# Kernel optimization log

Hardware: AMD Instinct MI355X
Metric: run time of the kernel (lower is better)

The kernel has to match this reference:

```python
import jax, jax.numpy as jnp
import numpy as np

EPS = 1e-12  # matches torch.nn.functional.normalize eps


def _normalize(x):
    n = jnp.sqrt(jnp.sum(x * x, axis=-1, keepdims=True))
    return x / jnp.maximum(n, EPS)


def setup_inputs() -> dict:
    key = jax.random.key(0)
    k1, k2, k3 = jax.random.split(key, 3)
    B, C, D = 1024, 32768, 512
    embeddings = jax.random.normal(k1, (B, D), dtype=jnp.float32)
    proxies = jax.random.normal(k2, (C, D), dtype=jnp.float32) / 8.0
    labels = jax.random.randint(k3, (B,), 0, C, dtype=jnp.int64)
    return {"embeddings": embeddings, "proxies": proxies, "labels": labels}


def reference(embeddings, proxies, labels):
    # batch: [B, D], P: [C, D], both scaled to norm 3
    batch = 3.0 * _normalize(embeddings)
    P = 3.0 * _normalize(proxies)

    # Squared euclidean distances to ALL proxies via the expansion
    # ||b - p||^2 = ||b||^2 + ||p||^2 - 2 b.p  -> [B, C]
    b_sq = jnp.sum(batch * batch, axis=-1, keepdims=True)      # [B, 1]
    p_sq = jnp.sum(P * P, axis=-1)                             # [C]
    dist = b_sq + p_sq[None, :] - 2.0 * (batch @ P.T)          # [B, C]

    B = batch.shape[0]
    rows = jnp.arange(B)
    pos_dist = dist[rows, labels]                              # [B]

    # logsumexp over negatives: mask out the positive class per row
    neg_scores = jnp.where(
        jnp.arange(dist.shape[1])[None, :] == labels[:, None],
        -jnp.inf,
        -dist,
    )
    neg_lse = jax.nn.logsumexp(neg_scores, axis=1)             # [B]

    return jnp.mean(pos_dist + neg_lse)
```

## Files before the change

kernel.cpp:

```cpp
#include <hip/hip_runtime.h>
#include <hip/hip_fp8.h>
#include <stdint.h>

#define D_DIM 512
#define B_ROWS 1024
#define C_ROWS 32768
#define NBLK (C_ROWS / 128)

typedef __attribute__((ext_vector_type(4))) float floatx4;

#define GLOBAL_AS __attribute__((address_space(1)))
#define LDS_AS __attribute__((address_space(3)))

__device__ inline void async_copy16(const unsigned char* g, unsigned char* l) {
    __builtin_amdgcn_global_load_lds((const GLOBAL_AS void*)g, (LDS_AS void*)l, 16, 0, 0);
}

__device__ inline unsigned char f2fp8(float x) {
    __hip_fp8_e4m3 t(x);
    return t.__x;
}
__device__ inline float fp8tof(unsigned char v) {
    __hip_fp8_e4m3 t;
    t.__x = v;
    return (float)t;
}

__global__ void norm_rows_kernel(const float* __restrict__ prox,
                                 const float* __restrict__ emb,
                                 unsigned char* __restrict__ Pq,
                                 unsigned char* __restrict__ Aq,
                                 float* __restrict__ rowsum,
                                 float* __restrict__ acc,
                                 unsigned* __restrict__ ticket) {
    if (blockIdx.x == 0) {
        for (int i = threadIdx.x; i < B_ROWS; i += 256) rowsum[i] = 0.f;
        if (threadIdx.x == 0) { *acc = 0.f; *ticket = 0u; }
    }
    const int wid = threadIdx.x >> 6;
    const int lane = threadIdx.x & 63;
    int row = blockIdx.x * 4 + wid;
    const float* src;
    unsigned char* dst;
    if (row < C_ROWS) {
        src = prox; dst = Pq;
    } else {
        row -= C_ROWS;
        src = emb; dst = Aq;
    }

    const float4* p = (const float4*)(src + (size_t)row * D_DIM + lane * 8);
    float4 v0 = p[0];
    float4 v1 = p[1];
    float ss = v0.x * v0.x + v0.y * v0.y + v0.z * v0.z + v0.w * v0.w +
               v1.x * v1.x + v1.y * v1.y + v1.z * v1.z + v1.w * v1.w;
#pragma unroll
    for (int off = 1; off < 64; off <<= 1) ss += __shfl_xor(ss, off);
    const float s = 3.0f * rsqrtf(ss);

    unsigned char q[8];
    q[0] = f2fp8(v0.x * s); q[1] = f2fp8(v0.y * s);
    q[2] = f2fp8(v0.z * s); q[3] = f2fp8(v0.w * s);
    q[4] = f2fp8(v1.x * s); q[5] = f2fp8(v1.y * s);
    q[6] = f2fp8(v1.z * s); q[7] = f2fp8(v1.w * s);
    uint2 packed;
    packed.x = (unsigned)q[0] | ((unsigned)q[1] << 8) |
               ((unsigned)q[2] << 16) | ((unsigned)q[3] << 24);
    packed.y = (unsigned)q[4] | ((unsigned)q[5] << 8) |
               ((unsigned)q[6] << 16) | ((unsigned)q[7] << 24);
    *(uint2*)(dst + (size_t)row * D_DIM + lane * 8) = packed;
}

__global__ void __launch_bounds__(256, 3)
gemm_lse_kernel(const unsigned char* __restrict__ A,
                const unsigned char* __restrict__ Bm,
                float* __restrict__ rowsum) {
    __shared__ unsigned char sA[128 * 128];
    __shared__ unsigned char sB[128 * 128];
    __shared__ float red[128];

    const int tid = threadIdx.x;
    const int wid = tid >> 6;
    const int lane = tid & 63;
    const int n0 = blockIdx.x * 128;
    const int m0 = blockIdx.y * 128;

    if (tid < 128) red[tid] = 0.f;

    const int r8 = lane >> 3;
    const int pg = lane & 7;
    const int gl = (pg - r8) & 7;
    const unsigned char* gA = A + (size_t)(m0 + wid * 32 + r8) * D_DIM + gl * 16;
    const unsigned char* gB = Bm + (size_t)(n0 + wid * 32 + r8) * D_DIM + gl * 16;
    unsigned char* lA = &sA[wid * 32 * 128 + lane * 16];
    unsigned char* lB = &sB[wid * 32 * 128 + lane * 16];

    const int wm = (wid >> 1) * 64;
    const int wn = (wid & 1) * 64;
    const int fr = lane & 15;
    const int quad = lane >> 4;

    floatx4 acc[4][4];
    const floatx4 zero = {0.f, 0.f, 0.f, 0.f};
#pragma unroll
    for (int i = 0; i < 4; ++i)
#pragma unroll
        for (int j = 0; j < 4; ++j) acc[i][j] = zero;

    for (int c = 0; c < 4; ++c) {
        const int kb = c * 128;
#pragma unroll
        for (int j = 0; j < 4; ++j) {
            async_copy16(gA + kb + j * 8 * D_DIM, lA + j * 8 * 128);
            async_copy16(gB + kb + j * 8 * D_DIM, lB + j * 8 * 128);
        }
        __syncthreads();

#pragma unroll
        for (int s = 0; s < 4; ++s) {
            const int off = (((2 * s + (quad >> 1) + fr) & 7) * 16) + (quad & 1) * 8;
            long af[4], bf[4];
#pragma unroll
            for (int t = 0; t < 4; ++t) {
                af[t] = *(const long*)&sA[(wm + t * 16 + fr) * 128 + off];
                bf[t] = *(const long*)&sB[(wn + t * 16 + fr) * 128 + off];
            }
#pragma unroll
            for (int ti = 0; ti < 4; ++ti)
#pragma unroll
                for (int tj = 0; tj < 4; ++tj)
                    acc[ti][tj] = __builtin_amdgcn_mfma_f32_16x16x32_fp8_fp8(
                        af[ti], bf[tj], acc[ti][tj], 0, 0, 0);
        }
        __syncthreads();
    }

#pragma unroll
    for (int ti = 0; ti < 4; ++ti) {
        float rs[4] = {0.f, 0.f, 0.f, 0.f};
#pragma unroll
        for (int tj = 0; tj < 4; ++tj)
#pragma unroll
            for (int r = 0; r < 4; ++r)
                rs[r] += __expf(2.0f * acc[ti][tj][r]);
#pragma unroll
        for (int r = 0; r < 4; ++r) {
            rs[r] += __shfl_xor(rs[r], 1);
            rs[r] += __shfl_xor(rs[r], 2);
            rs[r] += __shfl_xor(rs[r], 4);
            rs[r] += __shfl_xor(rs[r], 8);
        }
        if (fr == 0) {
#pragma unroll
            for (int r = 0; r < 4; ++r)
                atomicAdd(&red[wm + ti * 16 + quad * 4 + r], rs[r]);
        }
    }
    __syncthreads();
    if (tid < 128) atomicAdd(&rowsum[m0 + tid], red[tid]);
}

__global__ void finalize_kernel(const float* __restrict__ rowsum,
                                const unsigned char* __restrict__ A,
                                const unsigned char* __restrict__ Bm,
                                const int* __restrict__ labels,
                                float* __restrict__ acc,
                                unsigned* __restrict__ ticket,
                                float* __restrict__ out) {
    __shared__ float r4[4];
    const int tid = threadIdx.x;
    const int wid = tid >> 6;
    const int lane = tid & 63;
    const int b = blockIdx.x * 4 + wid;

    const int l = labels[b];
    uint2 ua = *(const uint2*)(A + (size_t)b * D_DIM + lane * 8);
    uint2 ub = *(const uint2*)(Bm + (size_t)l * D_DIM + lane * 8);
    const unsigned char* au = (const unsigned char*)&ua;
    const unsigned char* bu = (const unsigned char*)&ub;
    float d = 0.f;
#pragma unroll
    for (int j = 0; j < 8; ++j) d += fp8tof(au[j]) * fp8tof(bu[j]);
#pragma unroll
    for (int off = 1; off < 64; off <<= 1) d += __shfl_xor(d, off);

    if (lane == 0) {
        float p2 = 2.0f * d;
        r4[wid] = logf(rowsum[b] - __expf(p2)) - p2;
    }
    __syncthreads();
    if (tid == 0) {
        float bl = r4[0] + r4[1] + r4[2] + r4[3];
        atomicAdd(acc, bl);
        __threadfence();
        unsigned t = atomicAdd(ticket, 1u);
        if (t == 255u) {
            float total = atomicAdd(acc, 0.f);
            out[0] = total / (float)B_ROWS;
        }
    }
}

extern "C" void kernel_launch(void* const* d_in, const int* in_sizes, int n_in,
                              void* d_out, int out_size, void* d_ws, size_t ws_size,
                              hipStream_t stream) {
    const float* emb = (const float*)d_in[0];
    const float* prox = (const float*)d_in[1];
    const int* labels = (const int*)d_in[2];
    float* out = (float*)d_out;

    char* ws = (char*)d_ws;
    unsigned char* Pq = (unsigned char*)ws;
    unsigned char* Aq = Pq + (size_t)C_ROWS * D_DIM;
    float* rowsum = (float*)(Aq + (size_t)B_ROWS * D_DIM);
    float* acc = rowsum + B_ROWS;
    unsigned* ticket = (unsigned*)(acc + 1);

    norm_rows_kernel<<<(C_ROWS + B_ROWS) / 4, 256, 0, stream>>>(
        prox, emb, Pq, Aq, rowsum, acc, ticket);
    gemm_lse_kernel<<<dim3(NBLK, B_ROWS / 128), 256, 0, stream>>>(Aq, Pq, rowsum);
    finalize_kernel<<<B_ROWS / 4, 256, 0, stream>>>(
        rowsum, Aq, Pq, labels, acc, ticket, out);
}
```

Before: 142.2 us.

## Pre-swizzle A into MFMA fragment layout and load from registers, not LDS

The normalization kernel now writes the quantized embeddings in a layout that matches the MFMA fragments. The GEMM can then read A fragments straight from global memory into registers, double-buffered one k-step ahead, so A no longer goes through LDS. The B tile grows to a 256-wide K chunk, which halves the number of sync rounds, and the launch bound rises to 4 blocks per CU because LDS use drops. In exchange, A is now loaded per wave from global or L2 instead of being shared through LDS, and register pressure rises.

```diff
diff --git a/kernel.cpp b/kernel.cpp
--- a/kernel.cpp
+++ b/kernel.cpp
@@ -25,6 +25,7 @@
     t.__x = v;
     return (float)t;
 }
+
 
 __global__ void norm_rows_kernel(const float* __restrict__ prox,
                                  const float* __restrict__ emb,
@@ -41,12 +42,12 @@
     const int lane = threadIdx.x & 63;
     int row = blockIdx.x * 4 + wid;
     const float* src;
-    unsigned char* dst;
-    if (row < C_ROWS) {
-        src = prox; dst = Pq;
+    const bool is_prox = (row < C_ROWS);
+    if (is_prox) {
+        src = prox;
     } else {
         row -= C_ROWS;
-        src = emb; dst = Aq;
+        src = emb;
     }
 
     const float4* p = (const float4*)(src + (size_t)row * D_DIM + lane * 8);
@@ -68,38 +69,44 @@
                ((unsigned)q[2] << 16) | ((unsigned)q[3] << 24);
     packed.y = (unsigned)q[4] | ((unsigned)q[5] << 8) |
                ((unsigned)q[6] << 16) | ((unsigned)q[7] << 24);
-    *(uint2*)(dst + (size_t)row * D_DIM + lane * 8) = packed;
-}
-
-__global__ void __launch_bounds__(256, 3)
-gemm_lse_kernel(const unsigned char* __restrict__ A,
+
+    if (is_prox) {
+        *(uint2*)(Pq + (size_t)row * D_DIM + lane * 8) = packed;
+    } else {
+        const size_t u = ((size_t)(row >> 4) * 16 + (lane >> 2)) * 64 +
+                         (lane & 3) * 16 + (row & 15);
+        *(uint2*)(Aq + u * 8) = packed;
+    }
+}
+
+__global__ void __launch_bounds__(256, 4)
+gemm_lse_kernel(const unsigned char* __restrict__ Afrag,
                 const unsigned char* __restrict__ Bm,
                 float* __restrict__ rowsum) {
-    __shared__ unsigned char sA[128 * 128];
-    __shared__ unsigned char sB[128 * 128];
+    __shared__ unsigned char sB[128 * 256];
     __shared__ float red[128];
 
     const int tid = threadIdx.x;
     const int wid = tid >> 6;
     const int lane = tid & 63;
     const int n0 = blockIdx.x * 128;
-    const int m0 = blockIdx.y * 128;
+    const int m0t = blockIdx.y * 8;
 
     if (tid < 128) red[tid] = 0.f;
 
-    const int r8 = lane >> 3;
-    const int pg = lane & 7;
-    const int gl = (pg - r8) & 7;
-    const unsigned char* gA = A + (size_t)(m0 + wid * 32 + r8) * D_DIM + gl * 16;
-    const unsigned char* gB = Bm + (size_t)(n0 + wid * 32 + r8) * D_DIM + gl * 16;
-    unsigned char* lA = &sA[wid * 32 * 128 + lane * 16];
-    unsigned char* lB = &sB[wid * 32 * 128 + lane * 16];
-
-    const int wm = (wid >> 1) * 64;
+    const int r4 = lane >> 4;
+    const int pg = lane & 15;
+    unsigned char* lB = &sB[wid * 32 * 256 + lane * 16];
+
+    const int wmt = (wid >> 1) * 4;
+    const int wm = wmt * 16;
     const int wn = (wid & 1) * 64;
     const int fr = lane & 15;
     const int quad = lane >> 4;
 
+    const unsigned char* Abase =
+        Afrag + ((size_t)(m0t + wmt) * 16 * 64 + lane) * 8;
+
     floatx4 acc[4][4];
     const floatx4 zero = {0.f, 0.f, 0.f, 0.f};
 #pragma unroll
@@ -107,30 +114,43 @@
 #pragma unroll
         for (int j = 0; j < 4; ++j) acc[i][j] = zero;
 
-    for (int c = 0; c < 4; ++c) {
-        const int kb = c * 128;
-#pragma unroll
-        for (int j = 0; j < 4; ++j) {
-            async_copy16(gA + kb + j * 8 * D_DIM, lA + j * 8 * 128);
-            async_copy16(gB + kb + j * 8 * D_DIM, lB + j * 8 * 128);
+    long afb[2][4];
+#pragma unroll
+    for (int t = 0; t < 4; ++t)
+        afb[0][t] = *(const long*)(Abase + t * 8192);
+
+    for (int c = 0; c < 2; ++c) {
+#pragma unroll
+        for (int j = 0; j < 8; ++j) {
+            const int row = wid * 32 + j * 4 + r4;
+            const int gl = (pg - row) & 15;
+            async_copy16(Bm + (size_t)(n0 + row) * D_DIM + c * 256 + gl * 16,
+                         lB + j * 4 * 256);
         }
         __syncthreads();
 
 #pragma unroll
-        for (int s = 0; s < 4; ++s) {
-            const int off = (((2 * s + (quad >> 1) + fr) & 7) * 16) + (quad & 1) * 8;
-            long af[4], bf[4];
-#pragma unroll
-            for (int t = 0; t < 4; ++t) {
-                af[t] = *(const long*)&sA[(wm + t * 16 + fr) * 128 + off];
-                bf[t] = *(const long*)&sB[(wn + t * 16 + fr) * 128 + off];
+        for (int s = 0; s < 8; ++s) {
+            const int sidx = c * 8 + s;
+            const int cur = sidx & 1;
+            if (sidx < 15) {
+#pragma unroll
+                for (int t = 0; t < 4; ++t)
+                    afb[cur ^ 1][t] =
+                        *(const long*)(Abase + t * 8192 + (sidx + 1) * 512);
             }
+            const int off =
+                ((2 * s + (quad >> 1) + fr) & 15) * 16 + (quad & 1) * 8;
+            long bf[4];
+#pragma unroll
+            for (int t = 0; t < 4; ++t)
+                bf[t] = *(const long*)&sB[(wn + t * 16 + fr) * 256 + off];
 #pragma unroll
             for (int ti = 0; ti < 4; ++ti)
 #pragma unroll
                 for (int tj = 0; tj < 4; ++tj)
                     acc[ti][tj] = __builtin_amdgcn_mfma_f32_16x16x32_fp8_fp8(
-                        af[ti], bf[tj], acc[ti][tj], 0, 0, 0);
+                        afb[cur][ti], bf[tj], acc[ti][tj], 0, 0, 0);
         }
         __syncthreads();
     }
@@ -157,25 +177,27 @@
         }
     }
     __syncthreads();
-    if (tid < 128) atomicAdd(&rowsum[m0 + tid], red[tid]);
+    if (tid < 128) atomicAdd(&rowsum[m0t * 16 + tid], red[tid]);
 }
 
 __global__ void finalize_kernel(const float* __restrict__ rowsum,
-                                const unsigned char* __restrict__ A,
-                                const unsigned char* __restrict__ Bm,
+                                const unsigned char* __restrict__ Afrag,
+                                const unsigned char* __restrict__ Pq,
                                 const int* __restrict__ labels,
                                 float* __restrict__ acc,
                                 unsigned* __restrict__ ticket,
                                 float* __restrict__ out) {
-    __shared__ float r4[4];
+    __shared__ float r4s[4];
     const int tid = threadIdx.x;
     const int wid = tid >> 6;
     const int lane = tid & 63;
     const int b = blockIdx.x * 4 + wid;
 
     const int l = labels[b];
-    uint2 ua = *(const uint2*)(A + (size_t)b * D_DIM + lane * 8);
-    uint2 ub = *(const uint2*)(Bm + (size_t)l * D_DIM + lane * 8);
+    const size_t u = ((size_t)(b >> 4) * 16 + (lane >> 2)) * 64 +
+                     (lane & 3) * 16 + (b & 15);
+    uint2 ua = *(const uint2*)(Afrag + u * 8);
+    uint2 ub = *(const uint2*)(Pq + (size_t)l * D_DIM + lane * 8);
     const unsigned char* au = (const unsigned char*)&ua;
     const unsigned char* bu = (const unsigned char*)&ub;
     float d = 0.f;
@@ -186,11 +208,11 @@
 
     if (lane == 0) {
         float p2 = 2.0f * d;
-        r4[wid] = logf(rowsum[b] - __expf(p2)) - p2;
+        r4s[wid] = logf(rowsum[b] - __expf(p2)) - p2;
     }
     __syncthreads();
     if (tid == 0) {
-        float bl = r4[0] + r4[1] + r4[2] + r4[3];
+        float bl = r4s[0] + r4s[1] + r4s[2] + r4s[3];
         atomicAdd(acc, bl);
         __threadfence();
         unsigned t = atomicAdd(ticket, 1u);
```

Result: slower. 157.2 us (+10.6%).

## Pre-tile fp8 operands into MFMA fragment layout and replace atomics with partial sums

Applied to the files above, without the earlier changes.

The normalization kernel now writes quantized rows directly in a tiled layout that matches the MFMA fragment order, so the GEMM loads contiguous 16-byte chunks and reads 16-byte vectors from LDS with no swizzle arithmetic. Global atomicAdd into rowsum is replaced by per-block partial sums written to a workspace buffer, which the finalize kernel reduces. Launch bounds go from 3 to 4 blocks per CU. The change adds a larger partial buffer and ties every consumer to the new layout.

```diff
diff --git a/kernel.cpp b/kernel.cpp
--- a/kernel.cpp
+++ b/kernel.cpp
@@ -8,6 +8,7 @@
 #define NBLK (C_ROWS / 128)
 
 typedef __attribute__((ext_vector_type(4))) float floatx4;
+typedef __attribute__((ext_vector_type(2))) long longx2;
 
 #define GLOBAL_AS __attribute__((address_space(1)))
 #define LDS_AS __attribute__((address_space(3)))
@@ -26,17 +27,14 @@
     return (float)t;
 }
 
+
 __global__ void norm_rows_kernel(const float* __restrict__ prox,
                                  const float* __restrict__ emb,
                                  unsigned char* __restrict__ Pq,
                                  unsigned char* __restrict__ Aq,
-                                 float* __restrict__ rowsum,
                                  float* __restrict__ acc,
                                  unsigned* __restrict__ ticket) {
-    if (blockIdx.x == 0) {
-        for (int i = threadIdx.x; i < B_ROWS; i += 256) rowsum[i] = 0.f;
-        if (threadIdx.x == 0) { *acc = 0.f; *ticket = 0u; }
-    }
+    if (blockIdx.x == 0 && threadIdx.x == 0) { *acc = 0.f; *ticket = 0u; }
     const int wid = threadIdx.x >> 6;
     const int lane = threadIdx.x & 63;
     int row = blockIdx.x * 4 + wid;
@@ -68,35 +66,31 @@
                ((unsigned)q[2] << 16) | ((unsigned)q[3] << 24);
     packed.y = (unsigned)q[4] | ((unsigned)q[5] << 8) |
                ((unsigned)q[6] << 16) | ((unsigned)q[7] << 24);
-    *(uint2*)(dst + (size_t)row * D_DIM + lane * 8) = packed;
-}
-
-__global__ void __launch_bounds__(256, 3)
-gemm_lse_kernel(const unsigned char* __restrict__ A,
-                const unsigned char* __restrict__ Bm,
-                float* __restrict__ rowsum) {
-    __shared__ unsigned char sA[128 * 128];
-    __shared__ unsigned char sB[128 * 128];
+
+    const size_t u = ((size_t)(row >> 4) * 8 + (lane >> 3)) * 64 +
+                     (lane & 3) * 16 + (row & 15);
+    *(uint2*)(dst + u * 16 + ((lane >> 2) & 1) * 8) = packed;
+}
+
+__global__ void __launch_bounds__(256, 4)
+gemm_lse_kernel(const unsigned char* __restrict__ Aq,
+                const unsigned char* __restrict__ Bq,
+                float* __restrict__ part) {
+    __shared__ unsigned char sA[16384];
+    __shared__ unsigned char sB[16384];
     __shared__ float red[128];
 
     const int tid = threadIdx.x;
     const int wid = tid >> 6;
     const int lane = tid & 63;
-    const int n0 = blockIdx.x * 128;
-    const int m0 = blockIdx.y * 128;
+    const int n0t = blockIdx.x * 8;
+    const int m0t = blockIdx.y * 8;
 
     if (tid < 128) red[tid] = 0.f;
 
-    const int r8 = lane >> 3;
-    const int pg = lane & 7;
-    const int gl = (pg - r8) & 7;
-    const unsigned char* gA = A + (size_t)(m0 + wid * 32 + r8) * D_DIM + gl * 16;
-    const unsigned char* gB = Bm + (size_t)(n0 + wid * 32 + r8) * D_DIM + gl * 16;
-    unsigned char* lA = &sA[wid * 32 * 128 + lane * 16];
-    unsigned char* lB = &sB[wid * 32 * 128 + lane * 16];
-
-    const int wm = (wid >> 1) * 64;
-    const int wn = (wid & 1) * 64;
+    const int wmt = (wid >> 1) * 4;
+    const int wnt = (wid & 1) * 4;
+    const int wm = wmt * 16;
     const int fr = lane & 15;
     const int quad = lane >> 4;
 
@@ -108,29 +102,38 @@
         for (int j = 0; j < 4; ++j) acc[i][j] = zero;
 
     for (int c = 0; c < 4; ++c) {
-        const int kb = c * 128;
 #pragma unroll
         for (int j = 0; j < 4; ++j) {
-            async_copy16(gA + kb + j * 8 * D_DIM, lA + j * 8 * 128);
-            async_copy16(gB + kb + j * 8 * D_DIM, lB + j * 8 * 128);
+            const int tl = wid * 2 + (j >> 1);
+            const int sp = j & 1;
+            const size_t goA = (((size_t)(m0t + tl) * 8 + 2 * c + sp) * 64 + lane) * 16;
+            const size_t goB = (((size_t)(n0t + tl) * 8 + 2 * c + sp) * 64 + lane) * 16;
+            const int lo = ((tl * 2 + sp) * 64 + lane) * 16;
+            async_copy16(Aq + goA, &sA[lo]);
+            async_copy16(Bq + goB, &sB[lo]);
         }
         __syncthreads();
 
 #pragma unroll
-        for (int s = 0; s < 4; ++s) {
-            const int off = (((2 * s + (quad >> 1) + fr) & 7) * 16) + (quad & 1) * 8;
-            long af[4], bf[4];
+        for (int p = 0; p < 2; ++p) {
+            longx2 a2[4], b2[4];
 #pragma unroll
             for (int t = 0; t < 4; ++t) {
-                af[t] = *(const long*)&sA[(wm + t * 16 + fr) * 128 + off];
-                bf[t] = *(const long*)&sB[(wn + t * 16 + fr) * 128 + off];
+                a2[t] = *(const longx2*)&sA[(((wmt + t) * 2 + p) * 64 + lane) * 16];
+                b2[t] = *(const longx2*)&sB[(((wnt + t) * 2 + p) * 64 + lane) * 16];
             }
 #pragma unroll
             for (int ti = 0; ti < 4; ++ti)
 #pragma unroll
                 for (int tj = 0; tj < 4; ++tj)
                     acc[ti][tj] = __builtin_amdgcn_mfma_f32_16x16x32_fp8_fp8(
-                        af[ti], bf[tj], acc[ti][tj], 0, 0, 0);
+                        a2[ti][0], b2[tj][0], acc[ti][tj], 0, 0, 0);
+#pragma unroll
+            for (int ti = 0; ti < 4; ++ti)
+#pragma unroll
+                for (int tj = 0; tj < 4; ++tj)
+                    acc[ti][tj] = __builtin_amdgcn_mfma_f32_16x16x32_fp8_fp8(
+                        a2[ti][1], b2[tj][1], acc[ti][tj], 0, 0, 0);
         }
         __syncthreads();
     }
@@ -157,40 +160,53 @@
         }
     }
     __syncthreads();
-    if (tid < 128) atomicAdd(&rowsum[m0 + tid], red[tid]);
-}
-
-__global__ void finalize_kernel(const float* __restrict__ rowsum,
-                                const unsigned char* __restrict__ A,
-                                const unsigned char* __restrict__ Bm,
+    if (tid < 128)
+        part[(size_t)blockIdx.x * B_ROWS + m0t * 16 + tid] = red[tid];
+}
+
+__global__ void finalize_kernel(const float* __restrict__ part,
+                                const unsigned char* __restrict__ Aq,
+                                const unsigned char* __restrict__ Pq,
                                 const int* __restrict__ labels,
                                 float* __restrict__ acc,
                                 unsigned* __restrict__ ticket,
                                 float* __restrict__ out) {
-    __shared__ float r4[4];
+    __shared__ float r4s[4];
     const int tid = threadIdx.x;
     const int wid = tid >> 6;
     const int lane = tid & 63;
     const int b = blockIdx.x * 4 + wid;
 
+    float s = 0.f;
+#pragma unroll
+    for (int k = 0; k < 4; ++k)
+        s += part[(size_t)(lane * 4 + k) * B_ROWS + b];
+
     const int l = labels[b];
-    uint2 ua = *(const uint2*)(A + (size_t)b * D_DIM + lane * 8);
-    uint2 ub = *(const uint2*)(Bm + (size_t)l * D_DIM + lane * 8);
+    const size_t ua_u = ((size_t)(b >> 4) * 8 + (lane >> 3)) * 64 +
+                        (lane & 3) * 16 + (b & 15);
+    const size_t ub_u = ((size_t)(l >> 4) * 8 + (lane >> 3)) * 64 +
+                        (lane & 3) * 16 + (l & 15);
+    uint2 ua = *(const uint2*)(Aq + ua_u * 16 + ((lane >> 2) & 1) * 8);
+    uint2 ub = *(const uint2*)(Pq + ub_u * 16 + ((lane >> 2) & 1) * 8);
     const unsigned char* au = (const unsigned char*)&ua;
     const unsigned char* bu = (const unsigned char*)&ub;
     float d = 0.f;
 #pragma unroll
     for (int j = 0; j < 8; ++j) d += fp8tof(au[j]) * fp8tof(bu[j]);
 #pragma unroll
-    for (int off = 1; off < 64; off <<= 1) d += __shfl_xor(d, off);
+    for (int off = 1; off < 64; off <<= 1) {
+        s += __shfl_xor(s, off);
+        d += __shfl_xor(d, off);
+    }
 
     if (lane == 0) {
         float p2 = 2.0f * d;
-        r4[wid] = logf(rowsum[b] - __expf(p2)) - p2;
+        r4s[wid] = logf(s - __expf(p2)) - p2;
     }
     __syncthreads();
     if (tid == 0) {
-        float bl = r4[0] + r4[1] + r4[2] + r4[3];
+        float bl = r4s[0] + r4s[1] + r4s[2] + r4s[3];
         atomicAdd(acc, bl);
         __threadfence();
         unsigned t = atomicAdd(ticket, 1u);
@@ -212,13 +228,13 @@
     char* ws = (char*)d_ws;
     unsigned char* Pq = (unsigned char*)ws;
     unsigned char* Aq = Pq + (size_t)C_ROWS * D_DIM;
-    float* rowsum = (float*)(Aq + (size_t)B_ROWS * D_DIM);
-    float* acc = rowsum + B_ROWS;
+    float* part = (float*)(Aq + (size_t)B_ROWS * D_DIM);
+    float* acc = part + (size_t)NBLK * B_ROWS;
     unsigned* ticket = (unsigned*)(acc + 1);
 
     norm_rows_kernel<<<(C_ROWS + B_ROWS) / 4, 256, 0, stream>>>(
-        prox, emb, Pq, Aq, rowsum, acc, ticket);
-    gemm_lse_kernel<<<dim3(NBLK, B_ROWS / 128), 256, 0, stream>>>(Aq, Pq, rowsum);
+        prox, emb, Pq, Aq, acc, ticket);
+    gemm_lse_kernel<<<dim3(NBLK, B_ROWS / 128), 256, 0, stream>>>(Aq, Pq, part);
     finalize_kernel<<<B_ROWS / 4, 256, 0, stream>>>(
-        rowsum, Aq, Pq, labels, acc, ticket, out);
-}
+        part, Aq, Pq, labels, acc, ticket, out);
+}
```

New measurement: 139.4 us. 2.0% less time.
